# Performance work log

Hardware: AMD Instinct MI355X
Metric: run time of the kernel (lower is better)

## Reference

```python
import jax, jax.numpy as jnp
import numpy as np

MAX_SEQ_LEN = 4096

def bigbird_block_rand_mask(from_seq_length, to_seq_length, from_block_size, to_block_size, num_rand_blocks, last_idx=-1):
    rand_attn = np.zeros((from_seq_length // from_block_size - 2, num_rand_blocks), dtype=np.int32)
    middle_seq = np.arange(1, to_seq_length // to_block_size - 1, dtype=np.int32)
    last = to_seq_length // to_block_size - 1
    if last_idx > 2 * to_block_size:
        last = last_idx // to_block_size - 1
    r = num_rand_blocks
    nfb = from_seq_length // from_block_size
    for i in range(1, nfb - 1):
        start = i - 2
        end = i
        if i == 1:
            rand_attn[i - 1, :] = np.random.permutation(middle_seq[2:last])[:r]
        elif i == 2:
            rand_attn[i - 1, :] = np.random.permutation(middle_seq[3:last])[:r]
        elif i == nfb - 3:
            rand_attn[i - 1, :] = np.random.permutation(middle_seq[:last])[:r]
        elif i == nfb - 2:
            rand_attn[i - 1, :] = np.random.permutation(middle_seq[:last])[:r]
        elif start > last:
            start = last
            rand_attn[i - 1, :] = np.random.permutation(middle_seq[:start])[:r]
        elif end + 1 == last:
            rand_attn[i - 1, :] = np.random.permutation(middle_seq[:start])[:r]
        else:
            rand_attn[i - 1, :] = np.random.permutation(np.concatenate((middle_seq[:start], middle_seq[end + 1:last])))[:r]
    return rand_attn

def full_bigbird_mask(from_seq_length, to_seq_length, from_block_size, to_block_size, rand_attn):
    attn_mask = np.zeros((MAX_SEQ_LEN, MAX_SEQ_LEN), dtype=np.int32)
    for i in range(1, from_seq_length // from_block_size - 1):
        attn_mask[i * from_block_size:(i + 1) * from_block_size, (i - 1) * to_block_size:(i + 2) * to_block_size] = 1
        for j in rand_attn[i - 1, :]:
            attn_mask[i * from_block_size:(i + 1) * from_block_size, j * to_block_size:(j + 1) * to_block_size] = 1
    attn_mask[:from_block_size, :] = 1
    attn_mask[:, :to_block_size] = 1
    attn_mask[:, -to_block_size:] = 1
    attn_mask[-from_block_size:, :] = 1
    return attn_mask[:from_seq_length, :to_seq_length].astype(bool)

def setup_inputs() -> dict:
    B, H, F, T, D = 2, 16, 1024, 1024, 64
    BS, R, SEED = 64, 3, 0
    np.random.seed(SEED)
    rand_attn = np.stack([
        bigbird_block_rand_mask(MAX_SEQ_LEN, MAX_SEQ_LEN, BS, BS, R, last_idx=1024)[:F // BS - 2]
        for _ in range(H)
    ], axis=0)
    mask = np.stack([full_bigbird_mask(F, T, BS, BS, rand_attn[h]) for h in range(H)], axis=0)
    attention_mask = jnp.asarray(mask[None].astype(np.float32))  # [1, H, F, T]
    key = jax.random.key(0)
    kq, kk, kv = jax.random.split(key, 3)
    return {
        'query_layer': jax.random.normal(kq, (B, H, F, D), dtype=jnp.float32),
        'key_layer': jax.random.normal(kk, (B, H, T, D), dtype=jnp.float32),
        'value_layer': jax.random.normal(kv, (B, H, T, D), dtype=jnp.float32),
        'attention_mask': attention_mask,
    }

def reference(query_layer, key_layer, value_layer, attention_mask):
    d = query_layer.shape[-1]
    scores = jnp.einsum('bnfh,bnth->bnft', query_layer, key_layer) * (1.0 / np.sqrt(float(d)))
    scores = scores + (1.0 - attention_mask) * -10000.0
    probs = jax.nn.softmax(scores, axis=-1)
    # [batch, from_seq, heads, size_per_head]
    return jnp.einsum('bnft,bnth->bfnh', probs, value_layer)
```

## Files before the change

kernel.cpp:

```cpp
#include <hip/hip_runtime.h>

typedef __attribute__((ext_vector_type(4))) float f32x4;
typedef __attribute__((ext_vector_type(8))) short bf16x8;
typedef _Float16 f16x8 __attribute__((ext_vector_type(8)));

#define MFMA16(a, b, c) __builtin_amdgcn_mfma_f32_16x16x32_f16((a), (b), (c), 0, 0, 0)
#define MFMABF(a, b, c) __builtin_amdgcn_mfma_f32_16x16x32_bf16((a), (b), (c), 0, 0, 0)

constexpr size_t TILE_FRAG_BYTES = 8192;
constexpr size_t NTILES = 512;
constexpr size_t ARR_S  = NTILES * TILE_FRAG_BYTES;
constexpr size_t WS_NEED = 2 * ARR_S;

__device__ __forceinline__ int swz_off(int row, int col) {
    return (row * 128 + col * 2) ^ ((row & 7) << 4);
}
__device__ __forceinline__ f16x8 ld_frag16(const char* tile, int row, int col) {
    return *(const f16x8*)(tile + swz_off(row, col));
}

__global__ __launch_bounds__(256) void bigbird_prepass(
    const float* __restrict__ K, const float* __restrict__ V,
    char* __restrict__ ws) {
    __shared__ float vf[64][66];
    const int tile = blockIdx.x;
    const int tid  = threadIdx.x;
    const float* Kt = K + (size_t)tile * 4096;
    const float* Vt = V + (size_t)tile * 4096;
    f16x8* Ko = (f16x8*)(ws + (size_t)tile * TILE_FRAG_BYTES);
    f16x8* Vo = (f16x8*)(ws + ARR_S + (size_t)tile * TILE_FRAG_BYTES);

    {
        const int row = tid >> 2;
        const int c0  = (tid & 3) << 4;
        const float* p = Vt + row * 64 + c0;
        f32x4 e0 = *(const f32x4*)p,       e1 = *(const f32x4*)(p + 4),
              e2 = *(const f32x4*)(p + 8), e3 = *(const f32x4*)(p + 12);
#pragma unroll
        for (int e = 0; e < 4; ++e) {
            vf[row][c0 + e] = e0[e];     vf[row][c0 + 4 + e] = e1[e];
            vf[row][c0 + 8 + e] = e2[e]; vf[row][c0 + 12 + e] = e3[e];
        }
    }
#pragma unroll
    for (int t = 0; t < 2; ++t) {
        int s = tid + t * 256;
        int f = s >> 6, lane = s & 63;
        int j = f >> 1, kk = f & 1;
        int l16 = lane & 15, g = lane >> 4;
        const float* p = Kt + (j * 16 + l16) * 64 + kk * 32 + g * 8;
        f32x4 a = *(const f32x4*)p;
        f32x4 c = *(const f32x4*)(p + 4);
        f16x8 kv;
#pragma unroll
        for (int e = 0; e < 4; ++e) {
            kv[e]     = (_Float16)a[e];
            kv[4 + e] = (_Float16)c[e];
        }
        Ko[s] = kv;
    }
    __syncthreads();
#pragma unroll
    for (int t = 0; t < 2; ++t) {
        int s = tid + t * 256;
        int f = s >> 6, lane = s & 63;
        int j = f >> 1, kk = f & 1;
        int l16 = lane & 15, g = lane >> 4;
        f16x8 vv;
#pragma unroll
        for (int e = 0; e < 8; ++e)
            vv[e] = (_Float16)vf[kk * 32 + g * 8 + e][j * 16 + l16];
        Vo[s] = vv;
    }
}

__global__ __launch_bounds__(256, 4) void bigbird_main(
    const float* __restrict__ Q, const float* __restrict__ M,
    const char* __restrict__ ws, float* __restrict__ Out) {
    constexpr int H = 16, F = 1024, D = 64;

    __shared__ char  p_sm[4][2048];
    __shared__ float O_sm[32][65];
    __shared__ float m_sm[2][32], l_sm[2][32];
    __shared__ int flags[16];
    __shared__ int list[16];
    __shared__ int ncnt;

    const int i0  = blockIdx.x;
    const int xcd = i0 & 7;
    const int q0  = i0 >> 3;
    const int grp = xcd * 4 + (q0 >> 5);
    const int sb  = q0 & 31;
    const int b   = grp >> 4;
    const int h   = grp & 15;
    const int bh  = grp;

    const int tid  = threadIdx.x;
    const int lane = tid & 63;
    const int w    = tid >> 6;
    const int ws_  = w & 1;
    const int wt   = w >> 1;
    const int g    = lane >> 4;
    const int l16  = lane & 15;

    if (tid < 16)
        flags[tid] = (M[((size_t)(h * 1024 + sb * 32)) * 1024 + tid * 64] > 0.5f) ? 1 : 0;

    f16x8 qf[2];
    {
        const float* qr = Q + ((size_t)bh * F + sb * 32 + ws_ * 16 + l16) * D;
#pragma unroll
        for (int kk = 0; kk < 2; ++kk) {
            const float* p = qr + kk * 32 + g * 8;
            f32x4 a = *(const f32x4*)p;
            f32x4 c = *(const f32x4*)(p + 4);
#pragma unroll
            for (int e = 0; e < 8; ++e)
                qf[kk][e] = (_Float16)((e < 4 ? a[e] : c[e - 4]) * 0.125f);
        }
    }
    __syncthreads();
    if (tid == 0) {
        int nn = 0;
        for (int t = 0; t < 16; ++t)
            if (flags[t]) list[nn++] = t;
        ncnt = nn;
    }
    __syncthreads();
    const int n = ncnt;

    f32x4 acc[4];
    float m_r[4], l_r[4];
#pragma unroll
    for (int j = 0; j < 4; ++j) acc[j] = f32x4{0.f, 0.f, 0.f, 0.f};
#pragma unroll
    for (int r = 0; r < 4; ++r) { m_r[r] = -1e30f; l_r[r] = 0.f; }

    const f16x8* Kbase = (const f16x8*)ws + (size_t)bh * 16 * 512;
    const f16x8* Vbase = (const f16x8*)(ws + ARR_S) + (size_t)bh * 16 * 512;
    char* pw = p_sm[w];

    for (int i = wt; i < n; i += 2) {
        const int tb = list[i];
        const f16x8* Kf = Kbase + (size_t)tb * 512;
        const f16x8* Vf = Vbase + (size_t)tb * 512;

        f16x8 kfr[4][2], vfr[4][2];
#pragma unroll
        for (int j = 0; j < 4; ++j)
#pragma unroll
            for (int kk = 0; kk < 2; ++kk) {
                kfr[j][kk] = Kf[(j * 2 + kk) * 64 + lane];
                vfr[j][kk] = Vf[(j * 2 + kk) * 64 + lane];
            }

        f32x4 s[4];
#pragma unroll
        for (int j = 0; j < 4; ++j) {
            s[j] = f32x4{0.f, 0.f, 0.f, 0.f};
#pragma unroll
            for (int kk = 0; kk < 2; ++kk)
                s[j] = MFMA16(qf[kk], kfr[j][kk], s[j]);
        }

        float rmax[4];
#pragma unroll
        for (int r = 0; r < 4; ++r)
            rmax[r] = fmaxf(fmaxf(s[0][r], s[1][r]), fmaxf(s[2][r], s[3][r]));
#pragma unroll
        for (int off = 1; off < 16; off <<= 1)
#pragma unroll
            for (int r = 0; r < 4; ++r)
                rmax[r] = fmaxf(rmax[r], __shfl_xor(rmax[r], off, 64));
        float alpha[4], psum[4];
#pragma unroll
        for (int r = 0; r < 4; ++r) {
            float mn = fmaxf(m_r[r], rmax[r]);
            alpha[r] = __expf(m_r[r] - mn);
            m_r[r]   = mn;
            psum[r]  = 0.f;
        }
#pragma unroll
        for (int j = 0; j < 4; ++j)
#pragma unroll
            for (int r = 0; r < 4; ++r) {
                float pe = __expf(s[j][r] - m_r[r]);
                s[j][r] = pe;
                psum[r] += pe;
            }
#pragma unroll
        for (int off = 1; off < 16; off <<= 1)
#pragma unroll
            for (int r = 0; r < 4; ++r)
                psum[r] += __shfl_xor(psum[r], off, 64);
#pragma unroll
        for (int r = 0; r < 4; ++r)
            l_r[r] = l_r[r] * alpha[r] + psum[r];
#pragma unroll
        for (int j = 0; j < 4; ++j)
#pragma unroll
            for (int r = 0; r < 4; ++r)
                acc[j][r] *= alpha[r];

#pragma unroll
        for (int j = 0; j < 4; ++j)
#pragma unroll
            for (int r = 0; r < 4; ++r)
                *(_Float16*)(pw + swz_off(g * 4 + r, j * 16 + l16)) = (_Float16)s[j][r];
        asm volatile("s_waitcnt lgkmcnt(0)" ::: "memory");
        __builtin_amdgcn_sched_barrier(0);

#pragma unroll
        for (int kk = 0; kk < 2; ++kk) {
            f16x8 pa = ld_frag16(pw, l16, kk * 32 + g * 8);
#pragma unroll
            for (int jd = 0; jd < 4; ++jd)
                acc[jd] = MFMA16(pa, vfr[jd][kk], acc[jd]);
        }
    }

    if (l16 == 0) {
#pragma unroll
        for (int r = 0; r < 4; ++r) {
            int row = ws_ * 16 + g * 4 + r;
            m_sm[wt][row] = m_r[r];
            l_sm[wt][row] = l_r[r];
        }
    }
    __syncthreads();
    float inv_l[4];
#pragma unroll
    for (int r = 0; r < 4; ++r) {
        int row = ws_ * 16 + g * 4 + r;
        float m0 = m_sm[0][row], m1 = m_sm[1][row];
        float mm = fmaxf(m0, m1);
        float ll = l_sm[0][row] * __expf(m0 - mm) + l_sm[1][row] * __expf(m1 - mm);
        inv_l[r] = 1.0f / ll;
        float sc = __expf(m_r[r] - mm);
#pragma unroll
        for (int j = 0; j < 4; ++j) acc[j][r] *= sc;
    }
    if (wt == 0) {
#pragma unroll
        for (int j = 0; j < 4; ++j)
#pragma unroll
            for (int r = 0; r < 4; ++r)
                O_sm[ws_ * 16 + g * 4 + r][j * 16 + l16] = acc[j][r];
    }
    __syncthreads();
    if (wt == 1) {
#pragma unroll
        for (int j = 0; j < 4; ++j)
#pragma unroll
            for (int r = 0; r < 4; ++r)
                O_sm[ws_ * 16 + g * 4 + r][j * 16 + l16] += acc[j][r];
    }
    __syncthreads();

#pragma unroll
    for (int r = 0; r < 4; ++r) {
        int row = ws_ * 16 + g * 4 + r;
        int f = sb * 32 + row;
        float inv = inv_l[r];
        float* ob = Out + ((size_t)(b * F + f) * H + h) * D;
#pragma unroll
        for (int j2 = 0; j2 < 2; ++j2) {
            int col = wt * 32 + j2 * 16 + l16;
            ob[col] = O_sm[row][col] * inv;
        }
    }
}

__device__ __forceinline__ unsigned short f2bf(float x) {
    unsigned u = __builtin_bit_cast(unsigned, x);
    unsigned r = u + 0x7fffu + ((u >> 16) & 1u);
    return (unsigned short)(r >> 16);
}
__device__ __forceinline__ float bf2f(unsigned short h) {
    return __builtin_bit_cast(float, (unsigned)h << 16);
}
__device__ __forceinline__ bf16x8 ld_fragb(const char* tile, int row, int col) {
    return *(const bf16x8*)(tile + swz_off(row, col));
}
__device__ __forceinline__ void stage_rm_fb(const float* __restrict__ src,
                                            char* hi_t, char* lo_t, float scale) {
    const int tid = threadIdx.x;
    const int row = tid >> 2;
    const int c0  = (tid & 3) << 4;
    const float* p = src + row * 64 + c0;
    f32x4 vv[4] = { *(const f32x4*)(p), *(const f32x4*)(p + 4),
                    *(const f32x4*)(p + 8), *(const f32x4*)(p + 12) };
    bf16x8 h2[2], l2[2];
#pragma unroll
    for (int e = 0; e < 16; ++e) {
        float x = vv[e >> 2][e & 3] * scale;
        unsigned short hb = f2bf(x);
        unsigned short lb = f2bf(x - bf2f(hb));
        h2[e >> 3][e & 7] = (short)hb;
        l2[e >> 3][e & 7] = (short)lb;
    }
#pragma unroll
    for (int gi = 0; gi < 2; ++gi) {
        int off = swz_off(row, c0 + gi * 8);
        *(bf16x8*)(hi_t + off) = h2[gi];
        *(bf16x8*)(lo_t + off) = l2[gi];
    }
}
__device__ __forceinline__ void stage_tr_fb(const float* __restrict__ src,
                                            char* hi_t, char* lo_t) {
    const int tid = threadIdx.x;
    const int t  = tid >> 2;
    const int c0 = (tid & 3) << 4;
    const float* p = src + t * 64 + c0;
    f32x4 vv[4] = { *(const f32x4*)(p), *(const f32x4*)(p + 4),
                    *(const f32x4*)(p + 8), *(const f32x4*)(p + 12) };
#pragma unroll
    for (int e = 0; e < 16; ++e) {
        float x = vv[e >> 2][e & 3];
        unsigned short hb = f2bf(x);
        unsigned short lb = f2bf(x - bf2f(hb));
        int d = c0 + e;
        int off = (d * 128 + t * 2) ^ ((d & 7) << 4);
        *(unsigned short*)(hi_t + off) = hb;
        *(unsigned short*)(lo_t + off) = lb;
    }
}
__global__ __launch_bounds__(256) void bigbird_kernel_fb(
    const float* __restrict__ Q, const float* __restrict__ K,
    const float* __restrict__ V, const float* __restrict__ M,
    float* __restrict__ Out) {
    constexpr int H = 16, F = 1024, D = 64;
    __shared__ char kq_hi[8192];
    __shared__ char kq_lo[8192];
    __shared__ char vt_hi[8192];
    __shared__ char vt_lo[8192];
    __shared__ char p_smf[8192];
    __shared__ int flags[16];
    const int bid = blockIdx.x;
    const int fb  = bid & 15;
    const int h   = (bid >> 4) & 15;
    const int b   = bid >> 8;
    const int tid  = threadIdx.x;
    const int lane = tid & 63;
    const int w    = tid >> 6;
    const int g    = lane >> 4;
    const int l16  = lane & 15;
    if (tid < 16)
        flags[tid] = (M[(h * 1024 + fb * 64) * 1024 + tid * 64] > 0.5f) ? 1 : 0;
    const float* qb = Q + ((size_t)(b * H + h) * F + fb * 64) * D;
    stage_rm_fb(qb, kq_hi, kq_lo, 0.125f);
    __syncthreads();
    bf16x8 qh[2], ql[2];
#pragma unroll
    for (int kk = 0; kk < 2; ++kk) {
        qh[kk] = ld_fragb(kq_hi, w * 16 + l16, kk * 32 + g * 8);
        ql[kk] = ld_fragb(kq_lo, w * 16 + l16, kk * 32 + g * 8);
    }
    f32x4 acc[4];
    float m_r[4], l_r[4];
#pragma unroll
    for (int j = 0; j < 4; ++j) acc[j] = f32x4{0.f, 0.f, 0.f, 0.f};
#pragma unroll
    for (int r = 0; r < 4; ++r) { m_r[r] = -1e30f; l_r[r] = 0.f; }
    const float* kb = K + (size_t)(b * H + h) * 1024 * D;
    const float* vb = V + (size_t)(b * H + h) * 1024 * D;
    for (int tb = 0; tb < 16; ++tb) {
        if (!flags[tb]) continue;
        __syncthreads();
        stage_rm_fb(kb + tb * 64 * D, kq_hi, kq_lo, 1.0f);
        stage_tr_fb(vb + tb * 64 * D, vt_hi, vt_lo);
        __syncthreads();
        f32x4 s[4];
#pragma unroll
        for (int j = 0; j < 4; ++j) {
            s[j] = f32x4{0.f, 0.f, 0.f, 0.f};
#pragma unroll
            for (int kk = 0; kk < 2; ++kk) {
                bf16x8 bhf = ld_fragb(kq_hi, j * 16 + l16, kk * 32 + g * 8);
                bf16x8 blf = ld_fragb(kq_lo, j * 16 + l16, kk * 32 + g * 8);
                s[j] = MFMABF(qh[kk], bhf, s[j]);
                s[j] = MFMABF(qh[kk], blf, s[j]);
                s[j] = MFMABF(ql[kk], bhf, s[j]);
            }
        }
        float rmax[4];
#pragma unroll
        for (int r = 0; r < 4; ++r)
            rmax[r] = fmaxf(fmaxf(s[0][r], s[1][r]), fmaxf(s[2][r], s[3][r]));
#pragma unroll
        for (int off = 1; off < 16; off <<= 1)
#pragma unroll
            for (int r = 0; r < 4; ++r)
                rmax[r] = fmaxf(rmax[r], __shfl_xor(rmax[r], off, 64));
        float alpha[4], psum[4];
#pragma unroll
        for (int r = 0; r < 4; ++r) {
            float mn = fmaxf(m_r[r], rmax[r]);
            alpha[r] = __expf(m_r[r] - mn);
            m_r[r]   = mn;
            psum[r]  = 0.f;
        }
#pragma unroll
        for (int j = 0; j < 4; ++j)
#pragma unroll
            for (int r = 0; r < 4; ++r) {
                float pe = __expf(s[j][r] - m_r[r]);
                s[j][r] = pe;
                psum[r] += pe;
            }
#pragma unroll
        for (int off = 1; off < 16; off <<= 1)
#pragma unroll
            for (int r = 0; r < 4; ++r)
                psum[r] += __shfl_xor(psum[r], off, 64);
#pragma unroll
        for (int r = 0; r < 4; ++r)
            l_r[r] = l_r[r] * alpha[r] + psum[r];
#pragma unroll
        for (int j = 0; j < 4; ++j)
#pragma unroll
            for (int r = 0; r < 4; ++r)
                acc[j][r] *= alpha[r];
#pragma unroll
        for (int j = 0; j < 4; ++j)
#pragma unroll
            for (int r = 0; r < 4; ++r) {
                int row = w * 16 + g * 4 + r;
                *(unsigned short*)(p_smf + swz_off(row, j * 16 + l16)) = f2bf(s[j][r]);
            }
        __syncthreads();
#pragma unroll
        for (int kk = 0; kk < 2; ++kk) {
            bf16x8 pa = ld_fragb(p_smf, w * 16 + l16, kk * 32 + g * 8);
#pragma unroll
            for (int jd = 0; jd < 4; ++jd) {
                bf16x8 vh = ld_fragb(vt_hi, jd * 16 + l16, kk * 32 + g * 8);
                bf16x8 vl = ld_fragb(vt_lo, jd * 16 + l16, kk * 32 + g * 8);
                acc[jd] = MFMABF(pa, vh, acc[jd]);
                acc[jd] = MFMABF(pa, vl, acc[jd]);
            }
        }
    }
#pragma unroll
    for (int r = 0; r < 4; ++r) {
        float inv = 1.0f / l_r[r];
        int f = fb * 64 + w * 16 + g * 4 + r;
        float* ob = Out + ((size_t)(b * F + f) * H + h) * D;
#pragma unroll
        for (int jd = 0; jd < 4; ++jd)
            ob[jd * 16 + l16] = acc[jd][r] * inv;
    }
}

extern "C" void kernel_launch(void* const* d_in, const int* in_sizes, int n_in,
                              void* d_out, int out_size, void* d_ws, size_t ws_size,
                              hipStream_t stream) {
    const float* q = (const float*)d_in[0];
    const float* k = (const float*)d_in[1];
    const float* v = (const float*)d_in[2];
    const float* m = (const float*)d_in[3];
    float* out = (float*)d_out;
    if (ws_size >= WS_NEED) {
        bigbird_prepass<<<dim3(512), dim3(256), 0, stream>>>(k, v, (char*)d_ws);
        bigbird_main<<<dim3(1024), dim3(256), 0, stream>>>(q, m, (const char*)d_ws, out);
    } else {
        bigbird_kernel_fb<<<dim3(512), dim3(256), 0, stream>>>(q, k, v, m, out);
    }
}
```

Baseline: 39.08 us.

## Split key blocks into three chunks per row-block and combine partials in a separate kernel

```diff
diff --git a/kernel.cpp b/kernel.cpp
--- a/kernel.cpp
+++ b/kernel.cpp
@@ -10,7 +10,9 @@
 constexpr size_t TILE_FRAG_BYTES = 8192;
 constexpr size_t NTILES = 512;
 constexpr size_t ARR_S  = NTILES * TILE_FRAG_BYTES;
-constexpr size_t WS_NEED = 2 * ARR_S;
+constexpr size_t PART_O_OFF  = 16u << 20;
+constexpr size_t PART_ML_OFF = PART_O_OFF + 1536 * 16384;
+constexpr size_t WS_NEED = PART_ML_OFF + 1536 * 512;
 
 __device__ __forceinline__ int swz_off(int row, int col) {
     return (row * 128 + col * 2) ^ ((row & 7) << 4);
@@ -74,51 +76,32 @@
     }
 }
 
-__global__ __launch_bounds__(256, 4) void bigbird_main(
+__global__ __launch_bounds__(256) void bigbird_chunk(
     const float* __restrict__ Q, const float* __restrict__ M,
-    const char* __restrict__ ws, float* __restrict__ Out) {
+    char* __restrict__ ws) {
     constexpr int H = 16, F = 1024, D = 64;
 
-    __shared__ char  p_sm[4][2048];
-    __shared__ float O_sm[32][65];
-    __shared__ float m_sm[2][32], l_sm[2][32];
+    __shared__ char p_sm[4][2048];
     __shared__ int flags[16];
     __shared__ int list[16];
     __shared__ int ncnt;
 
-    const int i0  = blockIdx.x;
-    const int xcd = i0 & 7;
-    const int q0  = i0 >> 3;
-    const int grp = xcd * 4 + (q0 >> 5);
-    const int sb  = q0 & 31;
-    const int b   = grp >> 4;
-    const int h   = grp & 15;
-    const int bh  = grp;
+    const int bid = blockIdx.x;
+    const int rb  = bid & 511;
+    const int c   = bid >> 9;
+    const int bh  = rb >> 4;
+    const int fb  = rb & 15;
+    const int b   = bh >> 4;
+    const int h   = bh & 15;
 
     const int tid  = threadIdx.x;
     const int lane = tid & 63;
     const int w    = tid >> 6;
-    const int ws_  = w & 1;
-    const int wt   = w >> 1;
     const int g    = lane >> 4;
     const int l16  = lane & 15;
 
     if (tid < 16)
-        flags[tid] = (M[((size_t)(h * 1024 + sb * 32)) * 1024 + tid * 64] > 0.5f) ? 1 : 0;
-
-    f16x8 qf[2];
-    {
-        const float* qr = Q + ((size_t)bh * F + sb * 32 + ws_ * 16 + l16) * D;
-#pragma unroll
-        for (int kk = 0; kk < 2; ++kk) {
-            const float* p = qr + kk * 32 + g * 8;
-            f32x4 a = *(const f32x4*)p;
-            f32x4 c = *(const f32x4*)(p + 4);
-#pragma unroll
-            for (int e = 0; e < 8; ++e)
-                qf[kk][e] = (_Float16)((e < 4 ? a[e] : c[e - 4]) * 0.125f);
-        }
-    }
+        flags[tid] = (M[((size_t)(h * 1024 + fb * 64)) * 1024 + tid * 64] > 0.5f) ? 1 : 0;
     __syncthreads();
     if (tid == 0) {
         int nn = 0;
@@ -128,6 +111,24 @@
     }
     __syncthreads();
     const int n = ncnt;
+    const int s = (n + 2) / 3;
+    const int beg = c * s;
+    if (beg >= n) return;
+    const int end = min(beg + s, n);
+
+    f16x8 qf[2];
+    {
+        const float* qr = Q + ((size_t)bh * F + fb * 64 + w * 16 + l16) * D;
+#pragma unroll
+        for (int kk = 0; kk < 2; ++kk) {
+            const float* p = qr + kk * 32 + g * 8;
+            f32x4 a = *(const f32x4*)p;
+            f32x4 cc = *(const f32x4*)(p + 4);
+#pragma unroll
+            for (int e = 0; e < 8; ++e)
+                qf[kk][e] = (_Float16)((e < 4 ? a[e] : cc[e - 4]) * 0.125f);
+        }
+    }
 
     f32x4 acc[4];
     float m_r[4], l_r[4];
@@ -140,7 +141,7 @@
     const f16x8* Vbase = (const f16x8*)(ws + ARR_S) + (size_t)bh * 16 * 512;
     char* pw = p_sm[w];
 
-    for (int i = wt; i < n; i += 2) {
+    for (int i = beg; i < end; ++i) {
         const int tb = list[i];
         const f16x8* Kf = Kbase + (size_t)tb * 512;
         const f16x8* Vf = Vbase + (size_t)tb * 512;
@@ -154,19 +155,19 @@
                 vfr[j][kk] = Vf[(j * 2 + kk) * 64 + lane];
             }
 
-        f32x4 s[4];
+        f32x4 sv[4];
 #pragma unroll
         for (int j = 0; j < 4; ++j) {
-            s[j] = f32x4{0.f, 0.f, 0.f, 0.f};
+            sv[j] = f32x4{0.f, 0.f, 0.f, 0.f};
 #pragma unroll
             for (int kk = 0; kk < 2; ++kk)
-                s[j] = MFMA16(qf[kk], kfr[j][kk], s[j]);
+                sv[j] = MFMA16(qf[kk], kfr[j][kk], sv[j]);
         }
 
         float rmax[4];
 #pragma unroll
         for (int r = 0; r < 4; ++r)
-            rmax[r] = fmaxf(fmaxf(s[0][r], s[1][r]), fmaxf(s[2][r], s[3][r]));
+            rmax[r] = fmaxf(fmaxf(sv[0][r], sv[1][r]), fmaxf(sv[2][r], sv[3][r]));
 #pragma unroll
         for (int off = 1; off < 16; off <<= 1)
 #pragma unroll
@@ -184,8 +185,8 @@
         for (int j = 0; j < 4; ++j)
 #pragma unroll
             for (int r = 0; r < 4; ++r) {
-                float pe = __expf(s[j][r] - m_r[r]);
-                s[j][r] = pe;
+                float pe = __expf(sv[j][r] - m_r[r]);
+                sv[j][r] = pe;
                 psum[r] += pe;
             }
 #pragma unroll
@@ -206,7 +207,7 @@
         for (int j = 0; j < 4; ++j)
 #pragma unroll
             for (int r = 0; r < 4; ++r)
-                *(_Float16*)(pw + swz_off(g * 4 + r, j * 16 + l16)) = (_Float16)s[j][r];
+                *(_Float16*)(pw + swz_off(g * 4 + r, j * 16 + l16)) = (_Float16)sv[j][r];
         asm volatile("s_waitcnt lgkmcnt(0)" ::: "memory");
         __builtin_amdgcn_sched_barrier(0);
 
@@ -219,55 +220,84 @@
         }
     }
 
-    if (l16 == 0) {
-#pragma unroll
-        for (int r = 0; r < 4; ++r) {
-            int row = ws_ * 16 + g * 4 + r;
-            m_sm[wt][row] = m_r[r];
-            l_sm[wt][row] = l_r[r];
-        }
-    }
+    float* Op = (float*)(ws + PART_O_OFF + (size_t)(rb * 3 + c) * 16384);
+    float* ml = (float*)(ws + PART_ML_OFF + (size_t)(rb * 3 + c) * 512);
+#pragma unroll
+    for (int r = 0; r < 4; ++r) {
+        int row = w * 16 + g * 4 + r;
+#pragma unroll
+        for (int j = 0; j < 4; ++j)
+            Op[row * 64 + j * 16 + l16] = acc[j][r];
+        if (l16 == 0) {
+            ml[row]      = m_r[r];
+            ml[64 + row] = l_r[r];
+        }
+    }
+}
+
+__global__ __launch_bounds__(256) void bigbird_combine(
+    const float* __restrict__ M, const char* __restrict__ ws,
+    float* __restrict__ Out) {
+    constexpr int H = 16, F = 1024, D = 64;
+    __shared__ int flags[16];
+    __shared__ int ncnt;
+
+    const int rb = blockIdx.x;
+    const int bh = rb >> 4;
+    const int fb = rb & 15;
+    const int b  = bh >> 4;
+    const int h  = bh & 15;
+    const int tid = threadIdx.x;
+    const int row = tid >> 2;
+    const int q4  = tid & 3;
+
+    if (tid < 16)
+        flags[tid] = (M[((size_t)(h * 1024 + fb * 64)) * 1024 + tid * 64] > 0.5f) ? 1 : 0;
     __syncthreads();
-    float inv_l[4];
-#pragma unroll
-    for (int r = 0; r < 4; ++r) {
-        int row = ws_ * 16 + g * 4 + r;
-        float m0 = m_sm[0][row], m1 = m_sm[1][row];
-        float mm = fmaxf(m0, m1);
-        float ll = l_sm[0][row] * __expf(m0 - mm) + l_sm[1][row] * __expf(m1 - mm);
-        inv_l[r] = 1.0f / ll;
-        float sc = __expf(m_r[r] - mm);
-#pragma unroll
-        for (int j = 0; j < 4; ++j) acc[j][r] *= sc;
-    }
-    if (wt == 0) {
-#pragma unroll
-        for (int j = 0; j < 4; ++j)
-#pragma unroll
-            for (int r = 0; r < 4; ++r)
-                O_sm[ws_ * 16 + g * 4 + r][j * 16 + l16] = acc[j][r];
+    if (tid == 0) {
+        int nn = 0;
+        for (int t = 0; t < 16; ++t) nn += flags[t];
+        ncnt = nn;
     }
     __syncthreads();
-    if (wt == 1) {
-#pragma unroll
-        for (int j = 0; j < 4; ++j)
-#pragma unroll
-            for (int r = 0; r < 4; ++r)
-                O_sm[ws_ * 16 + g * 4 + r][j * 16 + l16] += acc[j][r];
-    }
-    __syncthreads();
-
-#pragma unroll
-    for (int r = 0; r < 4; ++r) {
-        int row = ws_ * 16 + g * 4 + r;
-        int f = sb * 32 + row;
-        float inv = inv_l[r];
-        float* ob = Out + ((size_t)(b * F + f) * H + h) * D;
-#pragma unroll
-        for (int j2 = 0; j2 < 2; ++j2) {
-            int col = wt * 32 + j2 * 16 + l16;
-            ob[col] = O_sm[row][col] * inv;
-        }
+    const int n = ncnt;
+    const int s = (n + 2) / 3;
+
+    const char* Obase  = ws + PART_O_OFF  + (size_t)rb * 3 * 16384;
+    const char* mlbase = ws + PART_ML_OFF + (size_t)rb * 3 * 512;
+
+    float Mx = -1e30f;
+#pragma unroll
+    for (int c = 0; c < 3; ++c)
+        if (c * s < n)
+            Mx = fmaxf(Mx, ((const float*)(mlbase + c * 512))[row]);
+
+    float L = 0.f;
+    f32x4 o[4] = { f32x4{0,0,0,0}, f32x4{0,0,0,0}, f32x4{0,0,0,0}, f32x4{0,0,0,0} };
+#pragma unroll
+    for (int c = 0; c < 3; ++c)
+        if (c * s < n) {
+            const float* ml = (const float*)(mlbase + c * 512);
+            float wgt = __expf(ml[row] - Mx);
+            L += ml[64 + row] * wgt;
+            const float* Op = (const float*)(Obase + c * 16384) + row * 64 + q4 * 16;
+#pragma unroll
+            for (int q = 0; q < 4; ++q) {
+                f32x4 v = *(const f32x4*)(Op + q * 4);
+#pragma unroll
+                for (int e = 0; e < 4; ++e) o[q][e] += v[e] * wgt;
+            }
+        }
+
+    float invL = 1.0f / L;
+    int f = fb * 64 + row;
+    float* ob = Out + ((size_t)(b * F + f) * H + h) * D + q4 * 16;
+#pragma unroll
+    for (int q = 0; q < 4; ++q) {
+        f32x4 v;
+#pragma unroll
+        for (int e = 0; e < 4; ++e) v[e] = o[q][e] * invL;
+        *(f32x4*)(ob + q * 4) = v;
     }
 }
 
@@ -462,7 +492,8 @@
     float* out = (float*)d_out;
     if (ws_size >= WS_NEED) {
         bigbird_prepass<<<dim3(512), dim3(256), 0, stream>>>(k, v, (char*)d_ws);
-        bigbird_main<<<dim3(1024), dim3(256), 0, stream>>>(q, m, (const char*)d_ws, out);
+        bigbird_chunk<<<dim3(1536), dim3(256), 0, stream>>>(q, m, (char*)d_ws);
+        bigbird_combine<<<dim3(512), dim3(256), 0, stream>>>(m, (const char*)d_ws, out);
     } else {
         bigbird_kernel_fb<<<dim3(512), dim3(256), 0, stream>>>(q, k, v, m, out);
     }
```

After: 52.74 us. 1.35x slower.
